# Optimization experiments

Hardware: AMD Instinct MI355X
Metric: run time of the kernel (lower is better)

Reference implementation:

```python
import jax, jax.numpy as jnp
import numpy as np

B, S, T, D, V = 512, 128, 128, 512, 128  # batch, enc len, dec steps (=longest_smi), dim_model, output_size


def setup_inputs() -> dict:
    key = jax.random.key(0)
    ks = jax.random.split(key, 17)
    sc = 0.05
    return {
        "e_all": jax.random.normal(ks[0], (B, S, D), jnp.float32),
        "e_h": jax.random.normal(ks[1], (1, B, D), jnp.float32),
        "e_c": jax.random.normal(ks[2], (1, B, D), jnp.float32),
        "target": jax.random.randint(ks[3], (B, T), 0, T),
        # params (Linear weights stored [in, out], y = x @ W + b)
        "E": jax.random.normal(ks[4], (T, D), jnp.float32) * sc,        # Embedding(longest_smi, D)
        "Wa": jax.random.normal(ks[5], (D, D), jnp.float32) * sc,
        "ba": jnp.zeros((D,), jnp.float32),
        "Ua": jax.random.normal(ks[6], (D, D), jnp.float32) * sc,
        "bu": jnp.zeros((D,), jnp.float32),
        "Va": jax.random.normal(ks[7], (D, 1), jnp.float32) * sc,
        "bv": jnp.zeros((1,), jnp.float32),
        "W_ih": jax.random.normal(ks[8], (2 * D, 4 * D), jnp.float32) * sc,
        "b_ih": jnp.zeros((4 * D,), jnp.float32),
        "W_hh": jax.random.normal(ks[9], (D, 4 * D), jnp.float32) * sc,
        "b_hh": jnp.zeros((4 * D,), jnp.float32),
        "W_out": jax.random.normal(ks[10], (D, V), jnp.float32) * sc,
        "b_out": jnp.zeros((V,), jnp.float32),
    }


def reference(e_all, e_h, e_c, target, E, Wa, ba, Ua, bu, Va, bv,
              W_ih, b_ih, W_hh, b_hh, W_out, b_out):
    Bb = e_all.shape[0]
    # teacher forcing: step 0 input is token 0 (SOS), then target[:, :-1]
    idx = jnp.concatenate([jnp.zeros((Bb, 1), target.dtype), target[:, :-1]], axis=1)  # [B,T]
    emb_all = E[idx]                       # [B,T,D] (dropout is identity in eval)
    keys_proj = e_all @ Ua + bu            # Ua(keys), loop-invariant  [B,S,D]
    h0, c0 = e_h[0], e_c[0]                # [B,D]

    def step(carry, emb):
        h, c = carry
        q = (h + c) @ Wa + ba                                   # [B,D]  Wa(query)
        s = jnp.tanh(q[:, None, :] + keys_proj) @ Va + bv       # [B,S,1]
        w = jax.nn.softmax(s[..., 0], axis=-1)                  # [B,S]
        ctx = jnp.einsum('bs,bsd->bd', w, e_all)                # [B,D]
        x = jnp.concatenate([emb, ctx], axis=-1)                # [B,2D]
        g = x @ W_ih + b_ih + h @ W_hh + b_hh                   # [B,4D], torch gate order i,f,g,o
        i_, f_, g_, o_ = jnp.split(g, 4, axis=-1)
        c2 = jax.nn.sigmoid(f_) * c + jax.nn.sigmoid(i_) * jnp.tanh(g_)
        h2 = jax.nn.sigmoid(o_) * jnp.tanh(c2)
        out = h2 @ W_out + b_out                                # [B,V]
        return (h2, c2), (out, w)

    _, (outs, attns) = jax.lax.scan(step, (h0, c0), jnp.swapaxes(emb_all, 0, 1))
    outputs = jax.nn.log_softmax(jnp.swapaxes(outs, 0, 1), axis=-1)  # [B,T,V]
    cross_attn = jnp.swapaxes(attns, 0, 1)                           # [B,T,S]
    return outputs, cross_attn
```

## Files before the change

### kernel.cpp

```cpp
#include <hip/hip_runtime.h>

#define B_ 512
#define S_ 128
#define T_ 128
#define D_ 512
#define V_ 128
#define LDW 72

typedef __attribute__((ext_vector_type(8))) short s16x8;
typedef __attribute__((ext_vector_type(4))) short s16x4;
typedef __attribute__((ext_vector_type(4))) float f32x4;

__device__ __forceinline__ float b2f(unsigned short h) {
    union { unsigned int u; float f; } x; x.u = ((unsigned int)h) << 16; return x.f;
}
__device__ __forceinline__ unsigned short f2b(float f) {
    union { float f; unsigned int u; } x; x.f = f;
    unsigned int u = x.u; u += 0x7FFFu + ((u >> 16) & 1u);
    return (unsigned short)(u >> 16);
}
#if __has_builtin(__builtin_amdgcn_rcpf)
__device__ __forceinline__ float rcp_f(float x) { return __builtin_amdgcn_rcpf(x); }
#else
__device__ __forceinline__ float rcp_f(float x) { return 1.0f / x; }
#endif
__device__ __forceinline__ float sigm(float x) { return rcp_f(1.0f + __expf(-x)); }
__device__ __forceinline__ float tanh_fast(float x) {
    float e = __expf(2.0f * fabsf(x));
    float r = 1.0f - 2.0f * rcp_f(e + 1.0f);
    return copysignf(r, x);
}

struct P {
    const int* target;
    const float* E; const float* bv; const float* ba; const float* bout;
    const short* vab;
    const short* ealb; const short* kpb;
    const short* WaT; const short* WehT; const short* WctxT; const short* WoutT;
    const float* bcat;
    short* qbf; short* xeh; short* ctxb; float* gp;
    short* hcbf; short* h2bf; float* cst;
    float* out_logits; float* out_attn;
};

struct AttnS { float scp[4][64]; float wbuf[S_]; float cpart[4][D_]; };
struct OutS  { short As[64][LDW]; short Bs[128][LDW]; };
struct PG2   { short As[128][LDW]; short Bs[64][LDW]; };
struct GateS { short As[64][LDW]; short Bs[64][LDW]; float gt[64][65]; };
union SharedC { OutS o; PG2 g; };

__device__ __forceinline__ void attn_phase(const P& p, AttnS& sh, int b, int step)
{
    const int t = threadIdx.x, lane = t & 63, wave = t >> 6;
    {
        const int sg = wave & 1, dh = wave >> 1;
        const int s = sg * 64 + lane;
        const short* kr = p.kpb + ((size_t)b * S_ + s) * D_ + dh * 256;
        const short* qv = p.qbf + (size_t)b * D_ + dh * 256;
        const short* vv = p.vab + dh * 256;
        float acc = 0.f;
        #pragma unroll 4
        for (int i = 0; i < 32; ++i) {
            s16x8 kv = *(const s16x8*)(kr + i * 8);
            s16x8 qk = *(const s16x8*)(qv + i * 8);
            s16x8 vk = *(const s16x8*)(vv + i * 8);
            #pragma unroll
            for (int j = 0; j < 8; ++j)
                acc += tanh_fast(b2f((unsigned short)qk[j]) + b2f((unsigned short)kv[j]))
                       * b2f((unsigned short)vk[j]);
        }
        sh.scp[wave][lane] = acc;
    }
    __syncthreads();
    if (wave == 0) {
        const float bvv = p.bv[0];
        float v0 = sh.scp[0][lane] + sh.scp[2][lane] + bvv;
        float v1 = sh.scp[1][lane] + sh.scp[3][lane] + bvv;
        float m = fmaxf(v0, v1);
        #pragma unroll
        for (int o = 32; o >= 1; o >>= 1) m = fmaxf(m, __shfl_xor(m, o));
        float e0 = __expf(v0 - m), e1 = __expf(v1 - m);
        float su = e0 + e1;
        #pragma unroll
        for (int o = 32; o >= 1; o >>= 1) su += __shfl_xor(su, o);
        float inv = rcp_f(su);
        float w0 = e0 * inv, w1 = e1 * inv;
        sh.wbuf[lane] = w0; sh.wbuf[lane + 64] = w1;
        float* ao = p.out_attn + ((size_t)b * T_ + step) * S_;
        ao[lane] = w0; ao[lane + 64] = w1;
    }
    __syncthreads();
    {
        const int d0 = lane * 8;
        f32x4 aA = {0.f,0.f,0.f,0.f}, aB = {0.f,0.f,0.f,0.f};
        const short* eb = p.ealb + (size_t)b * S_ * D_ + d0;
        #pragma unroll 4
        for (int i = 0; i < 32; ++i) {
            int s = wave * 32 + i;
            float wv = sh.wbuf[s];
            s16x8 ev = *(const s16x8*)(eb + (size_t)s * D_);
            #pragma unroll
            for (int j = 0; j < 4; ++j) aA[j] += wv * b2f((unsigned short)ev[j]);
            #pragma unroll
            for (int j = 0; j < 4; ++j) aB[j] += wv * b2f((unsigned short)ev[4 + j]);
        }
        *(f32x4*)&sh.cpart[wave][d0]     = aA;
        *(f32x4*)&sh.cpart[wave][d0 + 4] = aB;
    }
    __syncthreads();
    {
        int dd = t * 2;
        float v0 = sh.cpart[0][dd]   + sh.cpart[1][dd]   + sh.cpart[2][dd]   + sh.cpart[3][dd];
        float v1 = sh.cpart[0][dd+1] + sh.cpart[1][dd+1] + sh.cpart[2][dd+1] + sh.cpart[3][dd+1];
        short2 o2; o2.x = (short)f2b(v0); o2.y = (short)f2b(v1);
        *(short2*)(p.ctxb + (size_t)b * D_ + dd) = o2;
    }
}

__device__ __forceinline__ void pgate_phase(const P& p, PG2& sh, int bid2)
{
    const int t = threadIdx.x, lane = t & 63, wave = t >> 6;
    const int lrow = lane & 15, kq = lane >> 4;
    const int m0 = (bid2 >> 5) * 128, n0 = (bid2 & 31) * 64;
    const int K = 1024;
    f32x4 acc[2][4] = {};
    for (int k0 = 0; k0 < K; k0 += 64) {
        s16x8 va[4], vb[2];
        #pragma unroll
        for (int r = 0; r < 4; ++r) {
            int idx = r * 256 + t, row = idx >> 3, seg = idx & 7;
            va[r] = *(const s16x8*)(p.xeh + (size_t)(m0 + row) * K + k0 + seg * 8);
        }
        #pragma unroll
        for (int r = 0; r < 2; ++r) {
            int idx = r * 256 + t, row = idx >> 3, seg = idx & 7;
            vb[r] = *(const s16x8*)(p.WehT + (size_t)(n0 + row) * K + k0 + seg * 8);
        }
        __syncthreads();
        #pragma unroll
        for (int r = 0; r < 4; ++r) {
            int idx = r * 256 + t, row = idx >> 3, seg = idx & 7;
            *(s16x8*)(&sh.As[row][seg * 8]) = va[r];
        }
        #pragma unroll
        for (int r = 0; r < 2; ++r) {
            int idx = r * 256 + t, row = idx >> 3, seg = idx & 7;
            *(s16x8*)(&sh.Bs[row][seg * 8]) = vb[r];
        }
        __syncthreads();
        #pragma unroll
        for (int kk = 0; kk < 64; kk += 32) {
            s16x8 af[2], bf[4];
            af[0] = *(const s16x8*)(&sh.As[wave * 32 + lrow][kk + kq * 8]);
            af[1] = *(const s16x8*)(&sh.As[wave * 32 + 16 + lrow][kk + kq * 8]);
            #pragma unroll
            for (int f = 0; f < 4; ++f)
                bf[f] = *(const s16x8*)(&sh.Bs[f * 16 + lrow][kk + kq * 8]);
            #pragma unroll
            for (int m2 = 0; m2 < 2; ++m2)
                #pragma unroll
                for (int n2 = 0; n2 < 4; ++n2)
                    acc[m2][n2] = __builtin_amdgcn_mfma_f32_16x16x32_bf16(af[m2], bf[n2], acc[m2][n2], 0, 0, 0);
        }
    }
    #pragma unroll
    for (int m2 = 0; m2 < 2; ++m2)
        #pragma unroll
        for (int n2 = 0; n2 < 4; ++n2) {
            int col = n0 + n2 * 16 + lrow;
            float bvv = p.bcat[col];
            #pragma unroll
            for (int j = 0; j < 4; ++j) {
                int row = m0 + wave * 32 + m2 * 16 + kq * 4 + j;
                p.gp[(size_t)row * 2048 + col] = acc[m2][n2][j] + bvv;
            }
        }
}

__device__ __forceinline__ void fgate_phase(const P& p, GateS& sh, int bid, int step)
{
    const int t = threadIdx.x, lane = t & 63, wave = t >> 6;
    const int wr = wave >> 1, wc = wave & 1;
    const int lrow = lane & 15, kq = lane >> 4;
    const int srow = t >> 3, sseg = t & 7;
    const int m0 = (bid >> 5) * 64, n0 = (bid & 31) * 64;
    f32x4 acc[2][2] = {};
    for (int k0 = 0; k0 < 512; k0 += 64) {
        s16x8 va0 = *(const s16x8*)(p.ctxb + (size_t)(m0 + srow) * 512 + k0 + sseg * 8);
        s16x8 va1 = *(const s16x8*)(p.ctxb + (size_t)(m0 + srow + 32) * 512 + k0 + sseg * 8);
        s16x8 vb0 = *(const s16x8*)(p.WctxT + (size_t)(n0 + srow) * 512 + k0 + sseg * 8);
        s16x8 vb1 = *(const s16x8*)(p.WctxT + (size_t)(n0 + srow + 32) * 512 + k0 + sseg * 8);
        __syncthreads();
        *(s16x8*)(&sh.As[srow][sseg * 8]) = va0;
        *(s16x8*)(&sh.As[srow + 32][sseg * 8]) = va1;
        *(s16x8*)(&sh.Bs[srow][sseg * 8]) = vb0;
        *(s16x8*)(&sh.Bs[srow + 32][sseg * 8]) = vb1;
        __syncthreads();
        #pragma unroll
        for (int kk = 0; kk < 64; kk += 32) {
            s16x8 af0 = *(const s16x8*)(&sh.As[wr * 32 + lrow][kk + kq * 8]);
            s16x8 af1 = *(const s16x8*)(&sh.As[wr * 32 + 16 + lrow][kk + kq * 8]);
            s16x8 bf0 = *(const s16x8*)(&sh.Bs[wc * 32 + lrow][kk + kq * 8]);
            s16x8 bf1 = *(const s16x8*)(&sh.Bs[wc * 32 + 16 + lrow][kk + kq * 8]);
            acc[0][0] = __builtin_amdgcn_mfma_f32_16x16x32_bf16(af0, bf0, acc[0][0], 0, 0, 0);
            acc[0][1] = __builtin_amdgcn_mfma_f32_16x16x32_bf16(af0, bf1, acc[0][1], 0, 0, 0);
            acc[1][0] = __builtin_amdgcn_mfma_f32_16x16x32_bf16(af1, bf0, acc[1][0], 0, 0, 0);
            acc[1][1] = __builtin_amdgcn_mfma_f32_16x16x32_bf16(af1, bf1, acc[1][1], 0, 0, 0);
        }
    }
    #pragma unroll
    for (int m2 = 0; m2 < 2; ++m2)
        #pragma unroll
        for (int n2 = 0; n2 < 2; ++n2) {
            int cl = wc * 32 + n2 * 16 + lrow;
            #pragma unroll
            for (int j = 0; j < 4; ++j) {
                int rl = wr * 32 + m2 * 16 + kq * 4 + j;
                sh.gt[rl][cl] = acc[m2][n2][j] + p.gp[(size_t)(m0 + rl) * 2048 + n0 + cl];
            }
        }
    __syncthreads();
    const int rl4 = t >> 4, dl = t & 15;
    #pragma unroll
    for (int pass = 0; pass < 4; ++pass) {
        int row = pass * 16 + rl4;
        int b = m0 + row;
        int d = (n0 >> 2) + dl;
        float gi = sh.gt[row][dl * 4 + 0];
        float gf = sh.gt[row][dl * 4 + 1];
        float gg = sh.gt[row][dl * 4 + 2];
        float go = sh.gt[row][dl * 4 + 3];
        float cv = p.cst[(size_t)b * D_ + d];
        float c2 = sigm(gf) * cv + sigm(gi) * tanh_fast(gg);
        float h2 = sigm(go) * tanh_fast(c2);
        p.cst[(size_t)b * D_ + d] = c2;
        p.hcbf[(size_t)b * D_ + d] = (short)f2b(h2 + c2);
        p.h2bf[(size_t)b * D_ + d] = (short)f2b(h2);
        p.xeh[(size_t)b * 1024 + 512 + d] = (short)f2b(h2);
        int tok = p.target[b * T_ + step];
        p.xeh[(size_t)b * 1024 + d] = (short)f2b(p.E[(size_t)tok * D_ + d]);
    }
}

__device__ __forceinline__ void q_phase(const P& p, OutS& sh, int bid)
{
    const int t = threadIdx.x, lane = t & 63, wave = t >> 6;
    const int lrow = lane & 15, kq = lane >> 4;
    const int srow = t >> 3, sseg = t & 7;
    const int m0 = (bid >> 4) * 64, n0 = (bid & 15) * 32;
    f32x4 acc0 = {}, acc1 = {};
    for (int k0 = 0; k0 < 512; k0 += 64) {
        s16x8 va0 = *(const s16x8*)(p.hcbf + (size_t)(m0 + srow) * 512 + k0 + sseg * 8);
        s16x8 va1 = *(const s16x8*)(p.hcbf + (size_t)(m0 + srow + 32) * 512 + k0 + sseg * 8);
        int brow = n0 + (srow & 31);
        s16x8 vb0 = *(const s16x8*)(p.WaT + (size_t)brow * 512 + k0 + sseg * 8);
        __syncthreads();
        *(s16x8*)(&sh.As[srow][sseg * 8]) = va0;
        *(s16x8*)(&sh.As[srow + 32][sseg * 8]) = va1;
        if (srow < 32) *(s16x8*)(&sh.Bs[srow][sseg * 8]) = vb0;
        __syncthreads();
        #pragma unroll
        for (int kk = 0; kk < 64; kk += 32) {
            s16x8 af  = *(const s16x8*)(&sh.As[wave * 16 + lrow][kk + kq * 8]);
            s16x8 bf0 = *(const s16x8*)(&sh.Bs[lrow][kk + kq * 8]);
            s16x8 bf1 = *(const s16x8*)(&sh.Bs[16 + lrow][kk + kq * 8]);
            acc0 = __builtin_amdgcn_mfma_f32_16x16x32_bf16(af, bf0, acc0, 0, 0, 0);
            acc1 = __builtin_amdgcn_mfma_f32_16x16x32_bf16(af, bf1, acc1, 0, 0, 0);
        }
    }
    #pragma unroll
    for (int n2 = 0; n2 < 2; ++n2) {
        int col = n0 + n2 * 16 + lrow;
        float bvv = p.ba[col];
        f32x4 av = n2 ? acc1 : acc0;
        #pragma unroll
        for (int j = 0; j < 4; ++j) {
            int row = m0 + wave * 16 + kq * 4 + j;
            p.qbf[(size_t)row * 512 + col] = (short)f2b(av[j] + bvv);
        }
    }
}

__device__ __forceinline__ void out_phase(const P& p, OutS& sh, int obid, int step)
{
    const int t = threadIdx.x, lane = t & 63, wave = t >> 6;
    const int lrow = lane & 15, kq = lane >> 4;
    const int srow = t >> 3, sseg = t & 7;
    const int m0 = obid * 64;
    f32x4 acc[8] = {};
    for (int k0 = 0; k0 < 512; k0 += 64) {
        s16x8 va0 = *(const s16x8*)(p.h2bf + (size_t)(m0 + srow) * 512 + k0 + sseg * 8);
        s16x8 va1 = *(const s16x8*)(p.h2bf + (size_t)(m0 + srow + 32) * 512 + k0 + sseg * 8);
        s16x8 vb[4];
        #pragma unroll
        for (int p4 = 0; p4 < 4; ++p4)
            vb[p4] = *(const s16x8*)(p.WoutT + (size_t)(srow + p4 * 32) * 512 + k0 + sseg * 8);
        __syncthreads();
        *(s16x8*)(&sh.As[srow][sseg * 8]) = va0;
        *(s16x8*)(&sh.As[srow + 32][sseg * 8]) = va1;
        #pragma unroll
        for (int p4 = 0; p4 < 4; ++p4) *(s16x8*)(&sh.Bs[srow + p4 * 32][sseg * 8]) = vb[p4];
        __syncthreads();
        #pragma unroll
        for (int kk = 0; kk < 64; kk += 32) {
            s16x8 a = *(const s16x8*)(&sh.As[wave * 16 + lrow][kk + kq * 8]);
            #pragma unroll
            for (int f = 0; f < 8; ++f) {
                s16x8 b = *(const s16x8*)(&sh.Bs[f * 16 + lrow][kk + kq * 8]);
                acc[f] = __builtin_amdgcn_mfma_f32_16x16x32_bf16(a, b, acc[f], 0, 0, 0);
            }
        }
    }
    float colb[8];
    #pragma unroll
    for (int f = 0; f < 8; ++f) colb[f] = p.bout[f * 16 + lrow];
    #pragma unroll
    for (int j = 0; j < 4; ++j) {
        float v[8]; float mx = -1e30f;
        #pragma unroll
        for (int f = 0; f < 8; ++f) { v[f] = acc[f][j] + colb[f]; mx = fmaxf(mx, v[f]); }
        #pragma unroll
        for (int o = 1; o < 16; o <<= 1) mx = fmaxf(mx, __shfl_xor(mx, o));
        float sum = 0.f;
        #pragma unroll
        for (int f = 0; f < 8; ++f) sum += __expf(v[f] - mx);
        #pragma unroll
        for (int o = 1; o < 16; o <<= 1) sum += __shfl_xor(sum, o);
        float lse = mx + __logf(sum);
        int row = m0 + wave * 16 + kq * 4 + j;
        float* orow = p.out_logits + ((size_t)row * T_ + step) * V_;
        #pragma unroll
        for (int f = 0; f < 8; ++f) orow[f * 16 + lrow] = v[f] - lse;
    }
}

__global__ __launch_bounds__(256, 2) void kA(P p, int step) {
    __shared__ AttnS sh;
    attn_phase(p, sh, blockIdx.x, step);
}
__global__ __launch_bounds__(256, 2) void kB(P p, int step) {
    __shared__ GateS sh;
    fgate_phase(p, sh, blockIdx.x, step);
}
template<bool INIT>
__global__ __launch_bounds__(256, 2) void kC(P p, int step) {
    __shared__ SharedC sh;
    const int bid = blockIdx.x;
    if (bid < 128)       q_phase(p, sh.o, bid);
    else if (bid < 256)  pgate_phase(p, sh.g, bid - 128);
    else if (!INIT)      out_phase(p, sh.o, bid - 256, step);
}

__global__ __launch_bounds__(256)
void gemm64(const short* __restrict__ A, const short* __restrict__ Bt,
            const float* __restrict__ bias, short* __restrict__ Cp,
            int M, int N, int K)
{
    __shared__ __align__(16) short As[64][LDW];
    __shared__ __align__(16) short Bs[64][LDW];
    const int t = threadIdx.x;
    const int lane = t & 63, wave = t >> 6;
    const int wr = wave >> 1, wc = wave & 1;
    const int lrow = lane & 15, kq = lane >> 4;
    const int m0 = blockIdx.y * 64, n0 = blockIdx.x * 64;
    const int srow = t >> 3, sseg = t & 7;
    f32x4 acc[2][2] = {};
    for (int k0 = 0; k0 < K; k0 += 64) {
        s16x8 va0 = *(const s16x8*)(A + (size_t)(m0 + srow) * K + k0 + sseg * 8);
        s16x8 va1 = *(const s16x8*)(A + (size_t)(m0 + srow + 32) * K + k0 + sseg * 8);
        s16x8 vb0 = *(const s16x8*)(Bt + (size_t)(n0 + srow) * K + k0 + sseg * 8);
        s16x8 vb1 = *(const s16x8*)(Bt + (size_t)(n0 + srow + 32) * K + k0 + sseg * 8);
        __syncthreads();
        *(s16x8*)(&As[srow][sseg * 8]) = va0;
        *(s16x8*)(&As[srow + 32][sseg * 8]) = va1;
        *(s16x8*)(&Bs[srow][sseg * 8]) = vb0;
        *(s16x8*)(&Bs[srow + 32][sseg * 8]) = vb1;
        __syncthreads();
        for (int kk = 0; kk < 64; kk += 32) {
            s16x8 af[2], bf[2];
            af[0] = *(const s16x8*)(&As[wr * 32 + lrow][kk + kq * 8]);
            af[1] = *(const s16x8*)(&As[wr * 32 + 16 + lrow][kk + kq * 8]);
            bf[0] = *(const s16x8*)(&Bs[wc * 32 + lrow][kk + kq * 8]);
            bf[1] = *(const s16x8*)(&Bs[wc * 32 + 16 + lrow][kk + kq * 8]);
            for (int m2 = 0; m2 < 2; ++m2)
                for (int n2 = 0; n2 < 2; ++n2)
                    acc[m2][n2] = __builtin_amdgcn_mfma_f32_16x16x32_bf16(af[m2], bf[n2], acc[m2][n2], 0, 0, 0);
        }
    }
    for (int m2 = 0; m2 < 2; ++m2)
        for (int n2 = 0; n2 < 2; ++n2) {
            int col = n0 + wc * 32 + n2 * 16 + lrow;
            float bvv = bias ? bias[col] : 0.0f;
            for (int j = 0; j < 4; ++j) {
                int row = m0 + wr * 32 + m2 * 16 + kq * 4 + j;
                Cp[(size_t)row * N + col] = (short)f2b(acc[m2][n2][j] + bvv);
            }
        }
}

__global__ __launch_bounds__(256)
void init_state(const float* __restrict__ e_h, const float* __restrict__ e_c,
                float* __restrict__ c, short* __restrict__ hcbf,
                short* __restrict__ xeh, const float* __restrict__ E)
{
    int gid = blockIdx.x * 256 + threadIdx.x;
    int b = gid >> 9, d = gid & 511;
    float h0 = e_h[gid], c0 = e_c[gid];
    c[gid] = c0;
    hcbf[gid] = (short)f2b(h0 + c0);
    xeh[(size_t)b * 1024 + 512 + d] = (short)f2b(h0);
    xeh[(size_t)b * 1024 + d] = (short)f2b(E[d]);
}

__global__ __launch_bounds__(256)
void transpose_cast(const float* __restrict__ in, short* __restrict__ out,
                    int N, int ostride, int koff, int gate_perm)
{
    __shared__ float tile[64][65];
    int t = threadIdx.x;
    int n0 = blockIdx.x * 64, k0 = blockIdx.y * 64;
    int cc = t & 63, r4 = t >> 6;
    for (int i = 0; i < 16; ++i) {
        int r = i * 4 + r4;
        tile[r][cc] = in[(size_t)(k0 + r) * N + n0 + cc];
    }
    __syncthreads();
    for (int i = 0; i < 16; ++i) {
        int nr = i * 4 + r4;
        int ng = n0 + nr;
        int np = gate_perm ? ((ng & 511) * 4 + (ng >> 9)) : ng;
        out[(size_t)np * ostride + koff + k0 + cc] = (short)f2b(tile[cc][nr]);
    }
}

__global__ __launch_bounds__(256)
void cast_bf16_v4(const float* __restrict__ in, short* __restrict__ out, int n4)
{
    int i = blockIdx.x * 256 + threadIdx.x;
    int stride = gridDim.x * 256;
    for (; i < n4; i += stride) {
        f32x4 v = ((const f32x4*)in)[i];
        s16x4 o;
        for (int j = 0; j < 4; ++j) o[j] = (short)f2b(v[j]);
        ((s16x4*)out)[i] = o;
    }
}

__global__ __launch_bounds__(256)
void make_bcat(const float* __restrict__ b_ih, const float* __restrict__ b_hh, float* __restrict__ bcat)
{
    int i = blockIdx.x * 256 + threadIdx.x;
    if (i < 2048) {
        int np = (i & 511) * 4 + (i >> 9);
        bcat[np] = b_ih[i] + b_hh[i];
    }
}

extern "C" void kernel_launch(void* const* d_in, const int* in_sizes, int n_in,
                              void* d_out, int out_size, void* d_ws, size_t ws_size,
                              hipStream_t stream)
{
    const float* e_all  = (const float*)d_in[0];
    const float* e_h    = (const float*)d_in[1];
    const float* e_c    = (const float*)d_in[2];
    const int*   target = (const int*)d_in[3];
    const float* E      = (const float*)d_in[4];
    const float* Wa     = (const float*)d_in[5];
    const float* ba     = (const float*)d_in[6];
    const float* Ua     = (const float*)d_in[7];
    const float* bu     = (const float*)d_in[8];
    const float* Va     = (const float*)d_in[9];
    const float* bv     = (const float*)d_in[10];
    const float* W_ih   = (const float*)d_in[11];
    const float* b_ih   = (const float*)d_in[12];
    const float* W_hh   = (const float*)d_in[13];
    const float* b_hh   = (const float*)d_in[14];
    const float* W_out  = (const float*)d_in[15];
    const float* b_out  = (const float*)d_in[16];

    char* ws = (char*)d_ws;
    size_t off = 0;
    auto alloc = [&](size_t bytes) { void* p = ws + off; off += (bytes + 255) & ~255ull; return p; };
    short* ealb  = (short*)alloc((size_t)B_ * S_ * D_ * 2);
    short* kpb   = (short*)alloc((size_t)B_ * S_ * D_ * 2);
    short* WaT   = (short*)alloc((size_t)D_ * D_ * 2);
    short* UaT   = (short*)alloc((size_t)D_ * D_ * 2);
    short* WehT  = (short*)alloc((size_t)2048 * 1024 * 2);
    short* WctxT = (short*)alloc((size_t)2048 * 512 * 2);
    short* WoutT = (short*)alloc((size_t)V_ * D_ * 2);
    float* bcat  = (float*)alloc(2048 * 4);
    short* qbf   = (short*)alloc((size_t)B_ * D_ * 2);
    short* vab   = (short*)alloc((size_t)D_ * 2);
    short* xeh   = (short*)alloc((size_t)B_ * 1024 * 2);
    short* ctxb  = (short*)alloc((size_t)B_ * D_ * 2);
    float* gp    = (float*)alloc((size_t)B_ * 2048 * 4);
    short* hcbf  = (short*)alloc((size_t)B_ * D_ * 2);
    short* h2bf  = (short*)alloc((size_t)B_ * D_ * 2);
    float* cst   = (float*)alloc((size_t)B_ * D_ * 4);
    if (off > ws_size) return;

    float* out_logits = (float*)d_out;
    float* out_attn   = (float*)d_out + (size_t)B_ * T_ * V_;

    cast_bf16_v4<<<4096, 256, 0, stream>>>(e_all, ealb, B_ * S_ * D_ / 4);
    cast_bf16_v4<<<1,    256, 0, stream>>>(Va, vab, D_ / 4);
    transpose_cast<<<dim3(8, 8),  256, 0, stream>>>(Wa,  WaT,  512,  512, 0, 0);
    transpose_cast<<<dim3(8, 8),  256, 0, stream>>>(Ua,  UaT,  512,  512, 0, 0);
    transpose_cast<<<dim3(32, 8), 256, 0, stream>>>(W_ih,              WehT,  2048, 1024, 0,   1);
    transpose_cast<<<dim3(32, 8), 256, 0, stream>>>(W_ih + 512 * 2048, WctxT, 2048, 512,  0,   1);
    transpose_cast<<<dim3(32, 8), 256, 0, stream>>>(W_hh,              WehT,  2048, 1024, 512, 1);
    transpose_cast<<<dim3(2, 8),  256, 0, stream>>>(W_out, WoutT, 128, 512, 0, 0);
    make_bcat<<<8, 256, 0, stream>>>(b_ih, b_hh, bcat);
    gemm64<<<dim3(8, 1024), 256, 0, stream>>>(ealb, UaT, bu, kpb, B_ * S_, 512, 512);
    init_state<<<1024, 256, 0, stream>>>(e_h, e_c, cst, hcbf, xeh, E);

    P pp;
    pp.target = target; pp.E = E; pp.bv = bv; pp.ba = ba; pp.bout = b_out;
    pp.vab = vab;
    pp.ealb = ealb; pp.kpb = kpb; pp.WaT = WaT; pp.WehT = WehT; pp.WctxT = WctxT; pp.WoutT = WoutT;
    pp.bcat = bcat; pp.qbf = qbf; pp.xeh = xeh; pp.ctxb = ctxb; pp.gp = gp;
    pp.hcbf = hcbf; pp.h2bf = h2bf; pp.cst = cst;
    pp.out_logits = out_logits; pp.out_attn = out_attn;

    kC<true><<<256, 256, 0, stream>>>(pp, 0);

    for (int t = 0; t < T_; ++t) {
        kA<<<512, 256, 0, stream>>>(pp, t);
        kB<<<256, 256, 0, stream>>>(pp, t);
        kC<false><<<264, 256, 0, stream>>>(pp, t);
    }
    (void)n_in; (void)in_sizes; (void)out_size;
}
```

Before: 6.631 ms.

## Transpose key projections for coalesced attention loads, store gate partials in bf16

Adds a one-time transpose of the projected keys into a [B][D/8][S][8] layout, so adjacent lanes in the attention score loop read contiguous 16-byte chunks instead of strided rows. The precomputed gate partial buffer changes from fp32 to bf16 to halve its write and read traffic. The output projection for step t-1 moves from kC into kA of step t, with a final kernel for the last step, which rebalances work across launches. Costs are an extra workspace buffer, a preprocessing pass, and some precision loss in the gate partial sums.

```diff
diff --git a/kernel.cpp b/kernel.cpp
--- a/kernel.cpp
+++ b/kernel.cpp
@@ -35,10 +35,10 @@
     const int* target;
     const float* E; const float* bv; const float* ba; const float* bout;
     const short* vab;
-    const short* ealb; const short* kpb;
+    const short* ealb; const short* kpT;
     const short* WaT; const short* WehT; const short* WctxT; const short* WoutT;
     const float* bcat;
-    short* qbf; short* xeh; short* ctxb; float* gp;
+    short* qbf; short* xeh; short* ctxb; short* gpb;
     short* hcbf; short* h2bf; float* cst;
     float* out_logits; float* out_attn;
 };
@@ -47,6 +47,7 @@
 struct OutS  { short As[64][LDW]; short Bs[128][LDW]; };
 struct PG2   { short As[128][LDW]; short Bs[64][LDW]; };
 struct GateS { short As[64][LDW]; short Bs[64][LDW]; float gt[64][65]; };
+union SharedA { AttnS a; OutS o; };
 union SharedC { OutS o; PG2 g; };
 
 __device__ __forceinline__ void attn_phase(const P& p, AttnS& sh, int b, int step)
@@ -55,15 +56,15 @@
     {
         const int sg = wave & 1, dh = wave >> 1;
         const int s = sg * 64 + lane;
-        const short* kr = p.kpb + ((size_t)b * S_ + s) * D_ + dh * 256;
-        const short* qv = p.qbf + (size_t)b * D_ + dh * 256;
-        const short* vv = p.vab + dh * 256;
+        const short* kb = p.kpT + (size_t)b * (64 * 1024);
+        const short* qv = p.qbf + (size_t)b * D_;
         float acc = 0.f;
         #pragma unroll 4
         for (int i = 0; i < 32; ++i) {
-            s16x8 kv = *(const s16x8*)(kr + i * 8);
-            s16x8 qk = *(const s16x8*)(qv + i * 8);
-            s16x8 vk = *(const s16x8*)(vv + i * 8);
+            int g = dh * 32 + i;
+            s16x8 kv = *(const s16x8*)(kb + g * 1024 + s * 8);
+            s16x8 qk = *(const s16x8*)(qv + g * 8);
+            s16x8 vk = *(const s16x8*)(p.vab + g * 8);
             #pragma unroll
             for (int j = 0; j < 8; ++j)
                 acc += tanh_fast(b2f((unsigned short)qk[j]) + b2f((unsigned short)kv[j]))
@@ -172,7 +173,7 @@
             #pragma unroll
             for (int j = 0; j < 4; ++j) {
                 int row = m0 + wave * 32 + m2 * 16 + kq * 4 + j;
-                p.gp[(size_t)row * 2048 + col] = acc[m2][n2][j] + bvv;
+                p.gpb[(size_t)row * 2048 + col] = (short)f2b(acc[m2][n2][j] + bvv);
             }
         }
 }
@@ -216,7 +217,8 @@
             #pragma unroll
             for (int j = 0; j < 4; ++j) {
                 int rl = wr * 32 + m2 * 16 + kq * 4 + j;
-                sh.gt[rl][cl] = acc[m2][n2][j] + p.gp[(size_t)(m0 + rl) * 2048 + n0 + cl];
+                sh.gt[rl][cl] = acc[m2][n2][j]
+                              + b2f((unsigned short)p.gpb[(size_t)(m0 + rl) * 2048 + n0 + cl]);
             }
         }
     __syncthreads();
@@ -335,20 +337,24 @@
 }
 
 __global__ __launch_bounds__(256, 2) void kA(P p, int step) {
-    __shared__ AttnS sh;
-    attn_phase(p, sh, blockIdx.x, step);
+    __shared__ SharedA sh;
+    const int bid = blockIdx.x;
+    if (bid < 512)     attn_phase(p, sh.a, bid, step);
+    else if (step > 0) out_phase(p, sh.o, bid - 512, step - 1);
 }
 __global__ __launch_bounds__(256, 2) void kB(P p, int step) {
     __shared__ GateS sh;
     fgate_phase(p, sh, blockIdx.x, step);
 }
-template<bool INIT>
-__global__ __launch_bounds__(256, 2) void kC(P p, int step) {
+__global__ __launch_bounds__(256, 2) void kC(P p) {
     __shared__ SharedC sh;
     const int bid = blockIdx.x;
-    if (bid < 128)       q_phase(p, sh.o, bid);
-    else if (bid < 256)  pgate_phase(p, sh.g, bid - 128);
-    else if (!INIT)      out_phase(p, sh.o, bid - 256, step);
+    if (bid < 128) q_phase(p, sh.o, bid);
+    else           pgate_phase(p, sh.g, bid - 128);
+}
+__global__ __launch_bounds__(256, 2) void kOutLast(P p, int step) {
+    __shared__ OutS sh;
+    out_phase(p, sh, blockIdx.x, step);
 }
 
 __global__ __launch_bounds__(256)
@@ -396,6 +402,18 @@
                 Cp[(size_t)row * N + col] = (short)f2b(acc[m2][n2][j] + bvv);
             }
         }
+}
+
+__global__ __launch_bounds__(256)
+void transpose_kp(const short* __restrict__ in, short* __restrict__ out)
+{
+    const int b = blockIdx.x, t = threadIdx.x;
+    const size_t base = (size_t)b * (S_ * D_);
+    for (int k = t; k < 64 * S_; k += 256) {
+        int g = k >> 7, s = k & 127;
+        s16x8 v = *(const s16x8*)(in + base + (size_t)s * D_ + g * 8);
+        *(s16x8*)(out + base + (size_t)g * (S_ * 8) + s * 8) = v;
+    }
 }
 
 __global__ __launch_bounds__(256)
@@ -483,6 +501,7 @@
     auto alloc = [&](size_t bytes) { void* p = ws + off; off += (bytes + 255) & ~255ull; return p; };
     short* ealb  = (short*)alloc((size_t)B_ * S_ * D_ * 2);
     short* kpb   = (short*)alloc((size_t)B_ * S_ * D_ * 2);
+    short* kpT   = (short*)alloc((size_t)B_ * S_ * D_ * 2);
     short* WaT   = (short*)alloc((size_t)D_ * D_ * 2);
     short* UaT   = (short*)alloc((size_t)D_ * D_ * 2);
     short* WehT  = (short*)alloc((size_t)2048 * 1024 * 2);
@@ -493,7 +512,7 @@
     short* vab   = (short*)alloc((size_t)D_ * 2);
     short* xeh   = (short*)alloc((size_t)B_ * 1024 * 2);
     short* ctxb  = (short*)alloc((size_t)B_ * D_ * 2);
-    float* gp    = (float*)alloc((size_t)B_ * 2048 * 4);
+    short* gpb   = (short*)alloc((size_t)B_ * 2048 * 2);
     short* hcbf  = (short*)alloc((size_t)B_ * D_ * 2);
     short* h2bf  = (short*)alloc((size_t)B_ * D_ * 2);
     float* cst   = (float*)alloc((size_t)B_ * D_ * 4);
@@ -512,22 +531,24 @@
     transpose_cast<<<dim3(2, 8),  256, 0, stream>>>(W_out, WoutT, 128, 512, 0, 0);
     make_bcat<<<8, 256, 0, stream>>>(b_ih, b_hh, bcat);
     gemm64<<<dim3(8, 1024), 256, 0, stream>>>(ealb, UaT, bu, kpb, B_ * S_, 512, 512);
+    transpose_kp<<<512, 256, 0, stream>>>(kpb, kpT);
     init_state<<<1024, 256, 0, stream>>>(e_h, e_c, cst, hcbf, xeh, E);
 
     P pp;
     pp.target = target; pp.E = E; pp.bv = bv; pp.ba = ba; pp.bout = b_out;
     pp.vab = vab;
-    pp.ealb = ealb; pp.kpb = kpb; pp.WaT = WaT; pp.WehT = WehT; pp.WctxT = WctxT; pp.WoutT = WoutT;
-    pp.bcat = bcat; pp.qbf = qbf; pp.xeh = xeh; pp.ctxb = ctxb; pp.gp = gp;
+    pp.ealb = ealb; pp.kpT = kpT; pp.WaT = WaT; pp.WehT = WehT; pp.WctxT = WctxT; pp.WoutT = WoutT;
+    pp.bcat = bcat; pp.qbf = qbf; pp.xeh = xeh; pp.ctxb = ctxb; pp.gpb = gpb;
     pp.hcbf = hcbf; pp.h2bf = h2bf; pp.cst = cst;
     pp.out_logits = out_logits; pp.out_attn = out_attn;
 
-    kC<true><<<256, 256, 0, stream>>>(pp, 0);
+    kC<<<256, 256, 0, stream>>>(pp);
 
     for (int t = 0; t < T_; ++t) {
-        kA<<<512, 256, 0, stream>>>(pp, t);
+        kA<<<520, 256, 0, stream>>>(pp, t);
         kB<<<256, 256, 0, stream>>>(pp, t);
-        kC<false><<<264, 256, 0, stream>>>(pp, t);
-    }
+        kC<<<256, 256, 0, stream>>>(pp);
+    }
+    kOutLast<<<8, 256, 0, stream>>>(pp, T_ - 1);
     (void)n_in; (void)in_sizes; (void)out_size;
 }
```

Result: no change. 6.507 ms (-1.9%).
